# Kernel tuning notes

Hardware: AMD Instinct MI355X
Metric: run time of the kernel (lower is better)

Reference implementation:

```python
import jax, jax.numpy as jnp
import numpy as np

NUM_HEADS = 16
D_MODEL = 1024


def setup_inputs() -> dict:
    key = jax.random.key(0)
    k_x, k_q, k_k, k_v, k_o = jax.random.split(key, 5)
    scale = 1.0 / np.sqrt(D_MODEL)
    return {
        "x": jax.random.normal(k_x, (1, 4096, D_MODEL), dtype=jnp.float32),
        # nn.Linear weights stored as [out, in]; y = x @ W.T
        "W_Q": jax.random.normal(k_q, (D_MODEL, D_MODEL), dtype=jnp.float32) * scale,
        "W_K": jax.random.normal(k_k, (D_MODEL, D_MODEL), dtype=jnp.float32) * scale,
        "W_V": jax.random.normal(k_v, (D_MODEL, D_MODEL), dtype=jnp.float32) * scale,
        "W_O": jax.random.normal(k_o, (D_MODEL, D_MODEL), dtype=jnp.float32) * scale,
    }


def reference(x, W_Q, W_K, W_V, W_O):
    b, s, d = x.shape
    h = NUM_HEADS
    dh = d // h

    def split_heads(t):  # [b,s,d] -> [b,h,s,dh]
        return t.reshape(b, s, h, dh).transpose(0, 2, 1, 3)

    Q = split_heads(x @ W_Q.T)
    K = split_heads(x @ W_K.T)
    V = split_heads(x @ W_V.T)

    # explicit bmm -> softmax -> bmm (no masking: torch masked_fill was non-in-place)
    scores = jnp.einsum("bhqd,bhkd->bhqk", Q, K) / jnp.sqrt(jnp.float32(dh))
    weights = jax.nn.softmax(scores, axis=-1)
    out = jnp.einsum("bhqk,bhkd->bhqd", weights, V)  # [b,h,s,dh]
    out = out.transpose(0, 2, 1, 3).reshape(b, s, d)
    return out @ W_O.T
```

## Files before the change

### kernel.cpp

```cpp
#include <hip/hip_runtime.h>
#include <hip/hip_bf16.h>
#include <stdint.h>

typedef __bf16 bf16;
typedef __bf16 bf16x4 __attribute__((ext_vector_type(4)));
typedef __bf16 bf16x8 __attribute__((ext_vector_type(8)));
typedef float f32x4 __attribute__((ext_vector_type(4)));
typedef float f32x8 __attribute__((ext_vector_type(8)));
typedef float f32x16 __attribute__((ext_vector_type(16)));
typedef unsigned int u32;
typedef u32 u32x4 __attribute__((ext_vector_type(4)));

#define MFMA16(a, b, c) __builtin_amdgcn_mfma_f32_16x16x32_bf16((a), (b), (c), 0, 0, 0)
#define MFMA32(a, b, c) __builtin_amdgcn_mfma_f32_32x32x16_bf16((a), (b), (c), 0, 0, 0)

#if __has_builtin(__builtin_amdgcn_exp2f)
#define EXP2(x) __builtin_amdgcn_exp2f(x)
#else
#define EXP2(x) exp2f(x)
#endif

__device__ __forceinline__ void async_copy16(const void* g, void* l) {
    __builtin_amdgcn_global_load_lds(
        (const __attribute__((address_space(1))) uint32_t*)g,
        (__attribute__((address_space(3))) uint32_t*)l,
        16, 0, 0);
}

__device__ __forceinline__ u32 cvt_pk_bf16(float lo, float hi) {
    u32 r;
    asm("v_cvt_pk_bf16_f32 %0, %1, %2" : "=v"(r) : "v"(lo), "v"(hi));
    return r;
}

__global__ __launch_bounds__(256) void cast_all(const float* __restrict__ x,
                                                const float* __restrict__ wq,
                                                const float* __restrict__ wk,
                                                const float* __restrict__ wv,
                                                const float* __restrict__ wo,
                                                bf16* __restrict__ xb,
                                                bf16* __restrict__ wqk,
                                                bf16* __restrict__ wvb,
                                                bf16* __restrict__ wob,
                                                float qscale) {
    const int i = blockIdx.x * 256 + threadIdx.x;
    const float* src;
    bf16* dst;
    float scale = 1.0f;
    int j = i;
    if (j < 524288) {
        src = x; dst = xb;
    } else if ((j -= 524288) < 131072) {
        src = wq; dst = wqk; scale = qscale;
    } else if ((j -= 131072) < 131072) {
        src = wk; dst = wqk + 1024 * 1024;
    } else if ((j -= 131072) < 131072) {
        src = wv; dst = wvb;
    } else {
        j -= 131072;
        src = wo; dst = wob;
    }
    f32x8 v = *(const f32x8*)(src + (size_t)j * 8);
    bf16x8 o;
#pragma unroll
    for (int e = 0; e < 8; ++e) o[e] = (bf16)(v[e] * scale);
    *(bf16x8*)(dst + (size_t)j * 8) = o;
}

template <int BM, typename CT>
__global__ __launch_bounds__(256) void gemm_bt(const bf16* __restrict__ A,
                                               const bf16* __restrict__ B,
                                               CT* __restrict__ C,
                                               int M, int N, int K) {
    constexpr int MFR = BM / 32;
    __shared__ bf16 As[2][BM * 64];
    __shared__ bf16 Bs[2][128 * 64];
    const int tid = threadIdx.x;
    const int wave = tid >> 6, lane = tid & 63;
    const int l4 = lane >> 4, l15 = lane & 15;
    const int wr = wave >> 1, wc = wave & 1;
    const int rb = wr * (BM / 2);
    const size_t tM = (size_t)blockIdx.y * BM, tN = (size_t)blockIdx.x * 128;

    f32x4 acc[MFR][4] = {};

    const int srowA = (lane & 7) * 16;
    auto stage = [&](int buf, int kt) {
#pragma unroll
        for (int c = 0; c < BM / 32; ++c) {
            const int chunk = wave * (BM / 32) + c;
            const int row = chunk * 8 + (lane >> 3);
            const int scol = srowA ^ ((row & 7) << 4);
            const char* ga = (const char*)(A + (tM + row) * (size_t)K) + kt * 128 + scol;
            async_copy16(ga, (char*)&As[buf][0] + chunk * 1024);
        }
#pragma unroll
        for (int c = 0; c < 4; ++c) {
            const int chunk = wave * 4 + c;
            const int row = chunk * 8 + (lane >> 3);
            const int scol = srowA ^ ((row & 7) << 4);
            const char* gb = (const char*)(B + (tN + row) * (size_t)K) + kt * 128 + scol;
            async_copy16(gb, (char*)&Bs[buf][0] + chunk * 1024);
        }
    };
    auto lds_frag = [&](const bf16* base, int row, int colb) -> bf16x8 {
        const int addr = row * 128 + (colb ^ ((row & 7) << 4));
        return *(const bf16x8*)((const char*)base + addr);
    };

    const int nk = K >> 6;
    stage(0, 0);
    for (int kt = 0; kt < nk; ++kt) {
        const int buf = kt & 1;
        asm volatile("s_waitcnt vmcnt(0)" ::: "memory");
        __builtin_amdgcn_s_barrier();
        __builtin_amdgcn_sched_barrier(0);
        if (kt + 1 < nk) stage(buf ^ 1, kt + 1);

#pragma unroll
        for (int half = 0; half < 2; ++half) {
            bf16x8 aF[MFR], bF[4];
#pragma unroll
            for (int m = 0; m < MFR; ++m)
                aF[m] = lds_frag(&As[buf][0], rb + m * 16 + l15, half * 64 + l4 * 16);
#pragma unroll
            for (int n = 0; n < 4; ++n)
                bF[n] = lds_frag(&Bs[buf][0], wc * 64 + n * 16 + l15, half * 64 + l4 * 16);
            __builtin_amdgcn_s_setprio(1);
#pragma unroll
            for (int m = 0; m < MFR; ++m)
#pragma unroll
                for (int n = 0; n < 4; ++n)
                    acc[m][n] = MFMA16(aF[m], bF[n], acc[m][n]);
            __builtin_amdgcn_s_setprio(0);
        }
    }

#pragma unroll
    for (int m = 0; m < MFR; ++m) {
        const size_t row0 = tM + rb + m * 16 + l4 * 4;
#pragma unroll
        for (int n = 0; n < 4; ++n) {
            const size_t col = tN + wc * 64 + n * 16 + l15;
#pragma unroll
            for (int r = 0; r < 4; ++r) {
                C[(row0 + r) * (size_t)N + col] = (CT)acc[m][n][r];
            }
        }
    }
}

__global__ __launch_bounds__(256, 2) void attn_kernel(const bf16* __restrict__ qk,
                                                      const bf16* __restrict__ vt,
                                                      bf16* __restrict__ out) {
    const int b = blockIdx.x;
    const int h = (b & 7) * 2 + ((b >> 3) & 1);
    const int qb = b >> 4;
    const int tid = threadIdx.x;
    const int wave = tid >> 6, lane = tid & 63;
    const int l31 = lane & 31, hi = lane >> 5;

    __shared__ bf16 Kt[4][64 * 64];
    __shared__ bf16 Vs[4][64 * 64];

    const int qrow = qb * 128 + wave * 32 + l31;
    const bf16* qptr = qk + (size_t)qrow * 2048 + h * 64 + hi * 8;
    bf16x8 qf[4];
#pragma unroll
    for (int kd = 0; kd < 4; ++kd) qf[kd] = *(const bf16x8*)(qptr + kd * 16);
    asm volatile("s_waitcnt vmcnt(0)" ::: "memory");

    const bf16* Kg = qk + 1024 + h * 64;
    const bf16* Vg = vt + (size_t)(h * 64) * 4096;

    f32x16 o0 = {}, o1 = {};
    float lrun = 0.f;

    const int srow = (tid & 7) * 16;

    auto stage = [&](int buf, int t) {
        const int kv0 = t * 64;
#pragma unroll
        for (int c = 0; c < 2; ++c) {
            const int row = c * 32 + (tid >> 3);
            const int scol = srow ^ ((row & 7) << 4);
            const bf16* gk = Kg + (size_t)(kv0 + row) * 2048 + (scol >> 1);
            async_copy16(gk, (char*)&Kt[buf][0] + c * 4096 + wave * 1024);
            const bf16* gv = Vg + (size_t)row * 4096 + kv0 + (scol >> 1);
            async_copy16(gv, (char*)&Vs[buf][0] + c * 4096 + wave * 1024);
        }
    };

    auto lds_b128 = [&](const bf16* base, int row, int colb) -> bf16x8 {
        const int addr = row * 128 + (colb ^ ((row & 7) << 4));
        return *(const bf16x8*)((const char*)base + addr);
    };
    auto lds_b64 = [&](const bf16* base, int row, int colb) -> bf16x4 {
        const int addr = row * 128 + (colb ^ ((row & 7) << 4));
        return *(const bf16x4*)((const char*)base + addr);
    };

    stage(0, 0);
    stage(1, 1);
    for (int p = 0; p < 32; ++p) {
        asm volatile("s_waitcnt vmcnt(0)" ::: "memory");
        __builtin_amdgcn_s_barrier();
        __builtin_amdgcn_sched_barrier(0);
        if (p < 31) {
            stage((2 * p + 2) & 3, 2 * p + 2);
            stage((2 * p + 3) & 3, 2 * p + 3);
        }

#pragma unroll
        for (int tt = 0; tt < 2; ++tt) {
            const int t = 2 * p + tt;
            const int buf = t & 3;

            f32x16 s0 = {}, s1 = {};
            __builtin_amdgcn_s_setprio(1);
#pragma unroll
            for (int kd = 0; kd < 4; ++kd) {
                bf16x8 k0 = lds_b128(&Kt[buf][0], l31, hi * 16 + kd * 32);
                bf16x8 k1 = lds_b128(&Kt[buf][0], 32 + l31, hi * 16 + kd * 32);
                s0 = MFMA32(k0, qf[kd], s0);
                s1 = MFMA32(k1, qf[kd], s1);
            }
            __builtin_amdgcn_s_setprio(0);

            float p0[16], p1[16];
#pragma unroll
            for (int i = 0; i < 16; ++i) p0[i] = EXP2(s0[i]);
#pragma unroll
            for (int i = 0; i < 16; ++i) p1[i] = EXP2(s1[i]);
            {
                float a0 = 0.f, a1 = 0.f, a2 = 0.f, a3 = 0.f;
#pragma unroll
                for (int i = 0; i < 4; ++i) {
                    a0 += p0[i] + p0[8 + i];
                    a1 += p0[4 + i] + p0[12 + i];
                    a2 += p1[i] + p1[8 + i];
                    a3 += p1[4 + i] + p1[12 + i];
                }
                float ls = (a0 + a1) + (a2 + a3);
                ls += __shfl_xor(ls, 32, 64);
                lrun += ls;
            }

            u32 pw0[8], pw1[8];
#pragma unroll
            for (int t2 = 0; t2 < 8; ++t2) {
                pw0[t2] = cvt_pk_bf16(p0[2 * t2], p0[2 * t2 + 1]);
                pw1[t2] = cvt_pk_bf16(p1[2 * t2], p1[2 * t2 + 1]);
            }

            __builtin_amdgcn_s_setprio(1);
#pragma unroll
            for (int j = 0; j < 4; ++j) {
                const u32* pw = (j & 2) ? pw1 : pw0;
                const int o = (j & 1) * 4;
                u32x4 fr = {pw[o + 0], pw[o + 1], pw[o + 2], pw[o + 3]};
                const bf16x8 pf = __builtin_bit_cast(bf16x8, fr);
                const int c0 = 32 * j + 8 * hi;
                bf16x4 va = lds_b64(&Vs[buf][0], l31, c0);
                bf16x4 vb = lds_b64(&Vs[buf][0], l31, c0 + 16);
                bf16x4 vc = lds_b64(&Vs[buf][0], 32 + l31, c0);
                bf16x4 vd = lds_b64(&Vs[buf][0], 32 + l31, c0 + 16);
                const bf16x8 v0f = __builtin_shufflevector(va, vb, 0, 1, 2, 3, 4, 5, 6, 7);
                const bf16x8 v1f = __builtin_shufflevector(vc, vd, 0, 1, 2, 3, 4, 5, 6, 7);
                o0 = MFMA32(v0f, pf, o0);
                o1 = MFMA32(v1f, pf, o1);
            }
            __builtin_amdgcn_s_setprio(0);
        }
    }

    const float inv = 1.0f / lrun;
#pragma unroll
    for (int dt = 0; dt < 2; ++dt) {
        const f32x16& oo = dt ? o1 : o0;
#pragma unroll
        for (int g = 0; g < 4; ++g) {
            const u32 lo = cvt_pk_bf16(oo[4 * g + 0] * inv, oo[4 * g + 1] * inv);
            const u32 hi2 = cvt_pk_bf16(oo[4 * g + 2] * inv, oo[4 * g + 3] * inv);
            const int d0 = dt * 32 + 8 * g + 4 * hi;
            *(uint2*)(out + (size_t)qrow * 1024 + h * 64 + d0) = make_uint2(lo, hi2);
        }
    }
}

extern "C" void kernel_launch(void* const* d_in, const int* in_sizes, int n_in,
                              void* d_out, int out_size, void* d_ws, size_t ws_size,
                              hipStream_t stream) {
    const float* x = (const float*)d_in[0];
    const float* wq = (const float*)d_in[1];
    const float* wk = (const float*)d_in[2];
    const float* wv = (const float*)d_in[3];
    const float* wo = (const float*)d_in[4];
    float* out = (float*)d_out;

    char* ws = (char*)d_ws;
    bf16* xb = (bf16*)(ws);
    bf16* wqk = (bf16*)(ws + (8u << 20));
    bf16* wvb = (bf16*)(ws + (12u << 20));
    bf16* wob = (bf16*)(ws + (14u << 20));
    bf16* qkb = (bf16*)(ws + (16u << 20));
    bf16* vtb = (bf16*)(ws + (32u << 20));
    bf16* attno = xb;

    const float qscale = 0.125f * 1.44269504089f;
    cast_all<<<4096, 256, 0, stream>>>(x, wq, wk, wv, wo, xb, wqk, wvb, wob, qscale);

    gemm_bt<128, bf16><<<dim3(16, 32), 256, 0, stream>>>(xb, wqk, qkb, 4096, 2048, 1024);
    gemm_bt<64, bf16><<<dim3(32, 16), 256, 0, stream>>>(wvb, xb, vtb, 1024, 4096, 1024);
    attn_kernel<<<512, 256, 0, stream>>>(qkb, vtb, attno);
    gemm_bt<64, float><<<dim3(8, 64), 256, 0, stream>>>(attno, wob, out, 4096, 1024, 1024);
}
```

Baseline: 149.5 us.

## Split attention KV range across two blocks and merge with a normalization kernel

```diff
diff --git a/kernel.cpp b/kernel.cpp
--- a/kernel.cpp
+++ b/kernel.cpp
@@ -152,16 +152,18 @@
 
 __global__ __launch_bounds__(256, 2) void attn_kernel(const bf16* __restrict__ qk,
                                                       const bf16* __restrict__ vt,
-                                                      bf16* __restrict__ out) {
+                                                      bf16* __restrict__ opart,
+                                                      float* __restrict__ lpart) {
     const int b = blockIdx.x;
     const int h = (b & 7) * 2 + ((b >> 3) & 1);
-    const int qb = b >> 4;
+    const int qb = (b >> 4) & 31;
+    const int kvhalf = b >> 9;
     const int tid = threadIdx.x;
     const int wave = tid >> 6, lane = tid & 63;
     const int l31 = lane & 31, hi = lane >> 5;
 
-    __shared__ bf16 Kt[4][64 * 64];
-    __shared__ bf16 Vs[4][64 * 64];
+    __shared__ bf16 Kt[2][64 * 64];
+    __shared__ bf16 Vs[2][64 * 64];
 
     const int qrow = qb * 128 + wave * 32 + l31;
     const bf16* qptr = qk + (size_t)qrow * 2048 + h * 64 + hi * 8;
@@ -200,92 +202,101 @@
         return *(const bf16x4*)((const char*)base + addr);
     };
 
-    stage(0, 0);
-    stage(1, 1);
-    for (int p = 0; p < 32; ++p) {
+    const int kvbase = kvhalf * 32;
+    stage(0, kvbase);
+    for (int t0 = 0; t0 < 32; ++t0) {
+        const int buf = t0 & 1;
         asm volatile("s_waitcnt vmcnt(0)" ::: "memory");
         __builtin_amdgcn_s_barrier();
         __builtin_amdgcn_sched_barrier(0);
-        if (p < 31) {
-            stage((2 * p + 2) & 3, 2 * p + 2);
-            stage((2 * p + 3) & 3, 2 * p + 3);
-        }
-
-#pragma unroll
-        for (int tt = 0; tt < 2; ++tt) {
-            const int t = 2 * p + tt;
-            const int buf = t & 3;
-
-            f32x16 s0 = {}, s1 = {};
-            __builtin_amdgcn_s_setprio(1);
-#pragma unroll
-            for (int kd = 0; kd < 4; ++kd) {
-                bf16x8 k0 = lds_b128(&Kt[buf][0], l31, hi * 16 + kd * 32);
-                bf16x8 k1 = lds_b128(&Kt[buf][0], 32 + l31, hi * 16 + kd * 32);
-                s0 = MFMA32(k0, qf[kd], s0);
-                s1 = MFMA32(k1, qf[kd], s1);
+        if (t0 + 1 < 32) stage(buf ^ 1, kvbase + t0 + 1);
+
+        f32x16 s0 = {}, s1 = {};
+        __builtin_amdgcn_s_setprio(1);
+#pragma unroll
+        for (int kd = 0; kd < 4; ++kd) {
+            bf16x8 k0 = lds_b128(&Kt[buf][0], l31, hi * 16 + kd * 32);
+            bf16x8 k1 = lds_b128(&Kt[buf][0], 32 + l31, hi * 16 + kd * 32);
+            s0 = MFMA32(k0, qf[kd], s0);
+            s1 = MFMA32(k1, qf[kd], s1);
+        }
+        __builtin_amdgcn_s_setprio(0);
+
+        float p0[16], p1[16];
+#pragma unroll
+        for (int i = 0; i < 16; ++i) p0[i] = EXP2(s0[i]);
+#pragma unroll
+        for (int i = 0; i < 16; ++i) p1[i] = EXP2(s1[i]);
+        {
+            float a0 = 0.f, a1 = 0.f, a2 = 0.f, a3 = 0.f;
+#pragma unroll
+            for (int i = 0; i < 4; ++i) {
+                a0 += p0[i] + p0[8 + i];
+                a1 += p0[4 + i] + p0[12 + i];
+                a2 += p1[i] + p1[8 + i];
+                a3 += p1[4 + i] + p1[12 + i];
             }
-            __builtin_amdgcn_s_setprio(0);
-
-            float p0[16], p1[16];
-#pragma unroll
-            for (int i = 0; i < 16; ++i) p0[i] = EXP2(s0[i]);
-#pragma unroll
-            for (int i = 0; i < 16; ++i) p1[i] = EXP2(s1[i]);
-            {
-                float a0 = 0.f, a1 = 0.f, a2 = 0.f, a3 = 0.f;
-#pragma unroll
-                for (int i = 0; i < 4; ++i) {
-                    a0 += p0[i] + p0[8 + i];
-                    a1 += p0[4 + i] + p0[12 + i];
-                    a2 += p1[i] + p1[8 + i];
-                    a3 += p1[4 + i] + p1[12 + i];
-                }
-                float ls = (a0 + a1) + (a2 + a3);
-                ls += __shfl_xor(ls, 32, 64);
-                lrun += ls;
-            }
-
-            u32 pw0[8], pw1[8];
-#pragma unroll
-            for (int t2 = 0; t2 < 8; ++t2) {
-                pw0[t2] = cvt_pk_bf16(p0[2 * t2], p0[2 * t2 + 1]);
-                pw1[t2] = cvt_pk_bf16(p1[2 * t2], p1[2 * t2 + 1]);
-            }
-
-            __builtin_amdgcn_s_setprio(1);
-#pragma unroll
-            for (int j = 0; j < 4; ++j) {
-                const u32* pw = (j & 2) ? pw1 : pw0;
-                const int o = (j & 1) * 4;
-                u32x4 fr = {pw[o + 0], pw[o + 1], pw[o + 2], pw[o + 3]};
-                const bf16x8 pf = __builtin_bit_cast(bf16x8, fr);
-                const int c0 = 32 * j + 8 * hi;
-                bf16x4 va = lds_b64(&Vs[buf][0], l31, c0);
-                bf16x4 vb = lds_b64(&Vs[buf][0], l31, c0 + 16);
-                bf16x4 vc = lds_b64(&Vs[buf][0], 32 + l31, c0);
-                bf16x4 vd = lds_b64(&Vs[buf][0], 32 + l31, c0 + 16);
-                const bf16x8 v0f = __builtin_shufflevector(va, vb, 0, 1, 2, 3, 4, 5, 6, 7);
-                const bf16x8 v1f = __builtin_shufflevector(vc, vd, 0, 1, 2, 3, 4, 5, 6, 7);
-                o0 = MFMA32(v0f, pf, o0);
-                o1 = MFMA32(v1f, pf, o1);
-            }
-            __builtin_amdgcn_s_setprio(0);
-        }
-    }
-
-    const float inv = 1.0f / lrun;
+            float ls = (a0 + a1) + (a2 + a3);
+            ls += __shfl_xor(ls, 32, 64);
+            lrun += ls;
+        }
+
+        u32 pw0[8], pw1[8];
+#pragma unroll
+        for (int t2 = 0; t2 < 8; ++t2) {
+            pw0[t2] = cvt_pk_bf16(p0[2 * t2], p0[2 * t2 + 1]);
+            pw1[t2] = cvt_pk_bf16(p1[2 * t2], p1[2 * t2 + 1]);
+        }
+
+        __builtin_amdgcn_s_setprio(1);
+#pragma unroll
+        for (int j = 0; j < 4; ++j) {
+            const u32* pw = (j & 2) ? pw1 : pw0;
+            const int o = (j & 1) * 4;
+            u32x4 fr = {pw[o + 0], pw[o + 1], pw[o + 2], pw[o + 3]};
+            const bf16x8 pf = __builtin_bit_cast(bf16x8, fr);
+            const int c0 = 32 * j + 8 * hi;
+            bf16x4 va = lds_b64(&Vs[buf][0], l31, c0);
+            bf16x4 vb = lds_b64(&Vs[buf][0], l31, c0 + 16);
+            bf16x4 vc = lds_b64(&Vs[buf][0], 32 + l31, c0);
+            bf16x4 vd = lds_b64(&Vs[buf][0], 32 + l31, c0 + 16);
+            const bf16x8 v0f = __builtin_shufflevector(va, vb, 0, 1, 2, 3, 4, 5, 6, 7);
+            const bf16x8 v1f = __builtin_shufflevector(vc, vd, 0, 1, 2, 3, 4, 5, 6, 7);
+            o0 = MFMA32(v0f, pf, o0);
+            o1 = MFMA32(v1f, pf, o1);
+        }
+        __builtin_amdgcn_s_setprio(0);
+    }
+
+    bf16* ob = opart + (size_t)kvhalf * 4096 * 1024;
 #pragma unroll
     for (int dt = 0; dt < 2; ++dt) {
         const f32x16& oo = dt ? o1 : o0;
 #pragma unroll
         for (int g = 0; g < 4; ++g) {
-            const u32 lo = cvt_pk_bf16(oo[4 * g + 0] * inv, oo[4 * g + 1] * inv);
-            const u32 hi2 = cvt_pk_bf16(oo[4 * g + 2] * inv, oo[4 * g + 3] * inv);
+            const u32 lo = cvt_pk_bf16(oo[4 * g + 0], oo[4 * g + 1]);
+            const u32 hi2 = cvt_pk_bf16(oo[4 * g + 2], oo[4 * g + 3]);
             const int d0 = dt * 32 + 8 * g + 4 * hi;
-            *(uint2*)(out + (size_t)qrow * 1024 + h * 64 + d0) = make_uint2(lo, hi2);
-        }
-    }
+            *(uint2*)(ob + (size_t)qrow * 1024 + h * 64 + d0) = make_uint2(lo, hi2);
+        }
+    }
+    if (!hi) lpart[(size_t)kvhalf * 16 * 4096 + h * 4096 + qrow] = lrun;
+}
+
+__global__ __launch_bounds__(256) void attn_norm(const bf16* __restrict__ op1,
+                                                 const float* __restrict__ lpart,
+                                                 bf16* __restrict__ out ) {
+    const int i = blockIdx.x * 256 + threadIdx.x;
+    const int q = i >> 7, c0 = (i & 127) * 8;
+    const int h = c0 >> 6;
+    const float l = lpart[h * 4096 + q] + lpart[16 * 4096 + h * 4096 + q];
+    const float inv = 1.0f / l;
+    const bf16x8 a = *(const bf16x8*)(out + (size_t)i * 8);
+    const bf16x8 b = *(const bf16x8*)(op1 + (size_t)i * 8);
+    bf16x8 r;
+#pragma unroll
+    for (int e = 0; e < 8; ++e) r[e] = (bf16)(((float)a[e] + (float)b[e]) * inv);
+    *(bf16x8*)(out + (size_t)i * 8) = r;
 }
 
 extern "C" void kernel_launch(void* const* d_in, const int* in_sizes, int n_in,
@@ -302,9 +313,11 @@
     bf16* xb = (bf16*)(ws);
     bf16* wqk = (bf16*)(ws + (8u << 20));
     bf16* wvb = (bf16*)(ws + (12u << 20));
-    bf16* wob = (bf16*)(ws + (14u << 20));
     bf16* qkb = (bf16*)(ws + (16u << 20));
     bf16* vtb = (bf16*)(ws + (32u << 20));
+    bf16* wob = (bf16*)(ws + (40u << 20));
+    float* lpart = (float*)(ws + (42u << 20));
+    bf16* opart = xb;
     bf16* attno = xb;
 
     const float qscale = 0.125f * 1.44269504089f;
@@ -312,6 +325,7 @@
 
     gemm_bt<128, bf16><<<dim3(16, 32), 256, 0, stream>>>(xb, wqk, qkb, 4096, 2048, 1024);
     gemm_bt<64, bf16><<<dim3(32, 16), 256, 0, stream>>>(wvb, xb, vtb, 1024, 4096, 1024);
-    attn_kernel<<<512, 256, 0, stream>>>(qkb, vtb, attno);
+    attn_kernel<<<1024, 256, 0, stream>>>(qkb, vtb, opart, lpart);
+    attn_norm<<<2048, 256, 0, stream>>>(opart + (size_t)4096 * 1024, lpart, attno);
     gemm_bt<64, float><<<dim3(8, 64), 256, 0, stream>>>(attno, wob, out, 4096, 1024, 1024);
 }
```

Result: slower. 163.6 us (+9.4%).
